# Optimization experiments

Hardware: AMD Instinct MI355X
Metric: run time of the kernel (lower is better)

## Reference

```python
import jax, jax.numpy as jnp
import numpy as np

N_NODES, N_VARS, E = 100000, 50000, 640000
FEAT, H, L = 16, 128, 4
N_INT, K = 20000, 8  # integer vars with categorical heads, uniform domain size


def _mlp2(x, W1, b1, W2, b2):
    return jnp.maximum(x @ W1 + b1, 0.0) @ W2 + b2


def setup_inputs() -> dict:
    key = jax.random.key(0)
    ks = jax.random.split(key, 24)
    s = lambda i, shape, scale: jax.random.normal(ks[i], shape, dtype=jnp.float32) * scale
    inp = {
        "x": jax.random.normal(ks[0], (N_NODES, FEAT), dtype=jnp.float32),
        "edge_index": jax.random.randint(ks[1], (2, E), 0, N_NODES, dtype=jnp.int32).astype(jnp.int64),
        "num_vars": N_VARS,
        # NodeEmbedder (var / cons)
        "ve_W1": s(2, (FEAT, H), 0.25), "ve_b1": jnp.zeros((H,), jnp.float32),
        "ve_W2": s(3, (H, H), 0.09),   "ve_b2": jnp.zeros((H,), jnp.float32),
        "ce_W1": s(4, (FEAT, H), 0.25), "ce_b1": jnp.zeros((H,), jnp.float32),
        "ce_W2": s(5, (H, H), 0.09),   "ce_b2": jnp.zeros((H,), jnp.float32),
        # GCN backbone: stacked per-layer params
        "conv_W": s(6, (L, H, H), 0.09), "conv_b": jnp.zeros((L, H), jnp.float32),
        "ref_W1": s(7, (L, H, H), 0.09), "ref_b1": jnp.zeros((L, H), jnp.float32),
        "ref_W2": s(8, (L, H, H), 0.09), "ref_b2": jnp.zeros((L, H), jnp.float32),
        # Bernoulli head: H -> H//2 -> 1
        "bh_W1": s(9, (H, H // 2), 0.09), "bh_b1": jnp.zeros((H // 2,), jnp.float32),
        "bh_W2": s(10, (H // 2, 1), 0.12), "bh_b2": jnp.zeros((1,), jnp.float32),
        # Categorical heads: one Linear(H, K) per integer variable, batched
        "cat_W": s(11, (N_INT, H, K), 0.09),
        "cat_b": jnp.zeros((N_INT, K), jnp.float32),
    }
    return inp


def reference(x, edge_index, num_vars,
              ve_W1, ve_b1, ve_W2, ve_b2,
              ce_W1, ce_b1, ce_W2, ce_b2,
              conv_W, conv_b, ref_W1, ref_b1, ref_W2, ref_b2,
              bh_W1, bh_b1, bh_W2, bh_b2,
              cat_W, cat_b):
    N = x.shape[0]
    src, dst = edge_index[0], edge_index[1]
    # GCN normalization with self-loops: deg includes the self edge
    deg = jax.ops.segment_sum(jnp.ones((src.shape[0],), x.dtype), dst, num_segments=N) + 1.0
    dinv_sqrt = jax.lax.rsqrt(deg)
    enorm = dinv_sqrt[src] * dinv_sqrt[dst]      # [E]
    self_norm = (1.0 / deg)[:, None]             # [N,1] self-loop weight deg^-1

    var_h = _mlp2(x[:num_vars], ve_W1, ve_b1, ve_W2, ve_b2)
    cons_h = _mlp2(x[num_vars:], ce_W1, ce_b1, ce_W2, ce_b2)
    h = jnp.concatenate([var_h, cons_h], axis=0)  # [N,H]

    def gcn_conv(xin, W, b):
        hw = xin @ W
        agg = jax.ops.segment_sum(hw[src] * enorm[:, None], dst, num_segments=N)
        return agg + hw * self_norm + b

    def layer(xc, p):
        W, b, W1, b1, W2, b2 = p
        h_ = jnp.maximum(gcn_conv(xc, W, b), 0.0)
        return xc + _mlp2(h_, W1, b1, W2, b2), None

    h, _ = jax.lax.scan(layer, h, (conv_W, conv_b, ref_W1, ref_b1, ref_W2, ref_b2))

    vh = h[:num_vars]
    bern_logits = _mlp2(vh, bh_W1, bh_b1, bh_W2, bh_b2)[:, 0]          # [num_vars]
    n_int = cat_W.shape[0]
    cat_logits = jnp.einsum('nh,nhk->nk', vh[:n_int], cat_W) + cat_b    # [n_int,K]
    return bern_logits, cat_logits
```

## Files before the change

### kernel.cpp

```cpp
#include <hip/hip_runtime.h>
#include <hip/hip_bf16.h>


#define NN 100000
#define NV 50000
#define NE 640000
#define FEAT 16
#define HD 128
#define NL 4
#define NI 20000
#define KK 8
#define SCAN_BLK 98
#define LDP 136
#define WE_STRIDE (128*32 + 128*128)

typedef __hip_bfloat16 bf16;
typedef __attribute__((ext_vector_type(8))) short short8;
typedef __attribute__((ext_vector_type(4))) float f32x4;

static __device__ __forceinline__ ushort f2bu(float f) {
    __hip_bfloat16 b = __float2bfloat16(f);
    return *reinterpret_cast<ushort*>(&b);
}
static __device__ __forceinline__ float bu2f(ushort u) {
    __hip_bfloat16 b = *reinterpret_cast<__hip_bfloat16*>(&u);
    return __bfloat162float(b);
}

__global__ void k_deg_init(float* deg) {
    int i = blockIdx.x * blockDim.x + threadIdx.x;
    if (i < NN) deg[i] = 1.0f;
}

__global__ void k_deg_scatter(const int* __restrict__ ei, float* deg) {
    int e = blockIdx.x * blockDim.x + threadIdx.x;
    if (e < NE) atomicAdd(&deg[ei[NE + e]], 1.0f);
}

__global__ void k_deg_fin(const float* __restrict__ deg, float* dinv, float* selfn) {
    int i = blockIdx.x * blockDim.x + threadIdx.x;
    if (i < NN) {
        float d = deg[i];
        dinv[i]  = rsqrtf(d);
        selfn[i] = 1.0f / d;
    }
}

__global__ void k_scan_part(const float* __restrict__ deg, int* __restrict__ part) {
    __shared__ int s[256];
    const int t = threadIdx.x;
    const int i = blockIdx.x * 1024 + t * 4;
    int sum = 0;
#pragma unroll
    for (int j = 0; j < 4; ++j)
        if (i + j < NN) sum += (int)deg[i + j] - 1;
    s[t] = sum;
    __syncthreads();
    for (int off = 128; off > 0; off >>= 1) {
        if (t < off) s[t] += s[t + off];
        __syncthreads();
    }
    if (t == 0) part[blockIdx.x] = s[0];
}

__global__ void k_scan_mid(const int* __restrict__ part, int* __restrict__ blockoff,
                           int* __restrict__ row_ptr) {
    __shared__ int s[128];
    const int t = threadIdx.x;
    int v = (t < SCAN_BLK) ? part[t] : 0;
    s[t] = v;
    __syncthreads();
    for (int off = 1; off < 128; off <<= 1) {
        int u = (t >= off) ? s[t - off] : 0;
        __syncthreads();
        s[t] += u;
        __syncthreads();
    }
    if (t < SCAN_BLK) blockoff[t] = s[t] - v;
    if (t == 0) row_ptr[NN] = NE;
}

__global__ void k_scan_apply(const float* __restrict__ deg,
                             const int* __restrict__ blockoff,
                             int* __restrict__ row_ptr, int* __restrict__ cnt) {
    __shared__ int s[256];
    const int t = threadIdx.x;
    const int i = blockIdx.x * 1024 + t * 4;
    int c[4];
    int tsum = 0;
#pragma unroll
    for (int j = 0; j < 4; ++j) {
        c[j] = (i + j < NN) ? (int)deg[i + j] - 1 : 0;
        tsum += c[j];
    }
    s[t] = tsum;
    __syncthreads();
    for (int off = 1; off < 256; off <<= 1) {
        int u = (t >= off) ? s[t - off] : 0;
        __syncthreads();
        s[t] += u;
        __syncthreads();
    }
    int off = blockoff[blockIdx.x] + s[t] - tsum;
#pragma unroll
    for (int j = 0; j < 4; ++j) {
        if (i + j < NN) {
            row_ptr[i + j] = off;
            cnt[i + j] = 0;
            off += c[j];
        }
    }
}

__global__ void k_csr_fill(const int* __restrict__ ei,
                           const int* __restrict__ row_ptr, int* __restrict__ cnt,
                           const float* __restrict__ dinv,
                           int* __restrict__ col, float* __restrict__ wgt) {
    int e = blockIdx.x * blockDim.x + threadIdx.x;
    if (e >= NE) return;
    const int s = ei[e];
    const int d = ei[NE + e];
    const int pos = row_ptr[d] + atomicAdd(&cnt[d], 1);
    col[pos] = s;
    wgt[pos] = dinv[s] * dinv[d];
}

__global__ void k_wprep(const float* __restrict__ conv_W,
                        const float* __restrict__ ref_W1,
                        const float* __restrict__ ref_W2,
                        ushort* __restrict__ wt) {
    const int mat = blockIdx.x >> 7;
    const int j = blockIdx.x & 127;
    const int k = threadIdx.x;
    const float* src = (mat < 4) ? conv_W + (size_t)mat * HD * HD
                     : (mat < 8) ? ref_W1 + (size_t)(mat - 4) * HD * HD
                                 : ref_W2 + (size_t)(mat - 8) * HD * HD;
    wt[(size_t)mat * HD * HD + j * HD + k] = f2bu(src[k * HD + j]);
}

__global__ void k_wprep_embed(const float* __restrict__ vW1, const float* __restrict__ vW2,
                              const float* __restrict__ cW1, const float* __restrict__ cW2,
                              ushort* __restrict__ wte) {
    const int side = blockIdx.x >> 7;
    const int j = blockIdx.x & 127;
    const int k = threadIdx.x;
    const float* W1 = side ? cW1 : vW1;
    const float* W2 = side ? cW2 : vW2;
    ushort* o = wte + (size_t)side * WE_STRIDE;
    if (k < 32) o[j * 32 + k] = (k < FEAT) ? f2bu(W1[k * HD + j]) : (ushort)0;
    o[128 * 32 + j * HD + k] = f2bu(W2[k * HD + j]);
}

__global__ __launch_bounds__(256, 4) void k_embed_mfma(
        const float* __restrict__ x,
        const ushort* __restrict__ W1t, const float* __restrict__ b1,
        const ushort* __restrict__ W2t, const float* __restrict__ b2,
        const ushort* __restrict__ Wtc,
        int nbase, int nend,
        ushort* __restrict__ hb, ushort* __restrict__ hwb) {
    const int lane = threadIdx.x & 63, w = threadIdx.x >> 6;
    const int l15 = lane & 15, lg = lane >> 4;
    const int rowb = nbase + blockIdx.x * 128;
    __shared__ ushort hsm[128][LDP];

#pragma unroll
    for (int rt = 0; rt < 2; ++rt) {
        const int r = rowb + w * 32 + rt * 16 + l15;
        const int rc = r < nend ? r : nend - 1;
        short8 a = {0, 0, 0, 0, 0, 0, 0, 0};
        if (lg < 2) {
            const float* xp = x + (size_t)rc * FEAT + lg * 8;
#pragma unroll
            for (int i = 0; i < 8; ++i) a[i] = (short)f2bu(xp[i]);
        }
#pragma unroll
        for (int jt = 0; jt < 8; ++jt) {
            const float bv = b1[jt * 16 + l15];
            f32x4 acc = {bv, bv, bv, bv};
            short8 b = *reinterpret_cast<const short8*>(&W1t[(jt * 16 + l15) * 32 + lg * 8]);
            acc = __builtin_amdgcn_mfma_f32_16x16x32_bf16(a, b, acc, 0, 0, 0);
#pragma unroll
            for (int rr = 0; rr < 4; ++rr)
                hsm[w * 32 + rt * 16 + lg * 4 + rr][jt * 16 + l15] =
                    f2bu(fmaxf(acc[rr], 0.0f));
        }
    }
    __syncthreads();

#pragma unroll
    for (int rt = 0; rt < 2; ++rt) {
        f32x4 acc[8];
#pragma unroll
        for (int jt = 0; jt < 8; ++jt) {
            const float bv = b2[jt * 16 + l15];
            f32x4 v = {bv, bv, bv, bv};
            acc[jt] = v;
        }
#pragma unroll
        for (int ks = 0; ks < 4; ++ks) {
            short8 a = *reinterpret_cast<const short8*>(&hsm[w * 32 + rt * 16 + l15][ks * 32 + lg * 8]);
#pragma unroll
            for (int jt = 0; jt < 8; ++jt) {
                short8 b = *reinterpret_cast<const short8*>(&W2t[(jt * 16 + l15) * HD + ks * 32 + lg * 8]);
                acc[jt] = __builtin_amdgcn_mfma_f32_16x16x32_bf16(a, b, acc[jt], 0, 0, 0);
            }
        }
#pragma unroll
        for (int jt = 0; jt < 8; ++jt)
#pragma unroll
            for (int rr = 0; rr < 4; ++rr) {
                const int row = rowb + w * 32 + rt * 16 + lg * 4 + rr;
                const ushort hv = f2bu(acc[jt][rr]);
                if (row < nend) hb[(size_t)row * HD + jt * 16 + l15] = hv;
                hsm[w * 32 + rt * 16 + lg * 4 + rr][jt * 16 + l15] = hv;
            }
        f32x4 acc3[8];
        const f32x4 zero = {0.f, 0.f, 0.f, 0.f};
#pragma unroll
        for (int jt = 0; jt < 8; ++jt) acc3[jt] = zero;
#pragma unroll
        for (int ks = 0; ks < 4; ++ks) {
            short8 a = *reinterpret_cast<const short8*>(&hsm[w * 32 + rt * 16 + l15][ks * 32 + lg * 8]);
#pragma unroll
            for (int jt = 0; jt < 8; ++jt) {
                short8 b = *reinterpret_cast<const short8*>(&Wtc[(jt * 16 + l15) * HD + ks * 32 + lg * 8]);
                acc3[jt] = __builtin_amdgcn_mfma_f32_16x16x32_bf16(a, b, acc3[jt], 0, 0, 0);
            }
        }
#pragma unroll
        for (int jt = 0; jt < 8; ++jt)
#pragma unroll
            for (int rr = 0; rr < 4; ++rr) {
                const int row = rowb + w * 32 + rt * 16 + lg * 4 + rr;
                if (row < nend)
                    hwb[(size_t)row * HD + jt * 16 + l15] = f2bu(acc3[jt][rr]);
            }
    }
}

__global__ __launch_bounds__(256) void k_hw(
                     const ushort* __restrict__ hb, const ushort* __restrict__ Wt,
                     ushort* __restrict__ hwb) {
    const int lane = threadIdx.x & 63;
    const int w = threadIdx.x >> 6;
    const int row0 = blockIdx.x * 128 + w * 32;
    const int l15 = lane & 15, lg = lane >> 4;

    const f32x4 zero = {0.f, 0.f, 0.f, 0.f};
    f32x4 acc[2][8];
#pragma unroll
    for (int rt = 0; rt < 2; ++rt)
#pragma unroll
        for (int jt = 0; jt < 8; ++jt) acc[rt][jt] = zero;

#pragma unroll
    for (int ks = 0; ks < 4; ++ks) {
        short8 a[2];
#pragma unroll
        for (int rt = 0; rt < 2; ++rt) {
            int r = row0 + rt * 16 + l15;
            r = r < NN ? r : NN - 1;
            a[rt] = *reinterpret_cast<const short8*>(&hb[(size_t)r * HD + ks * 32 + lg * 8]);
        }
#pragma unroll
        for (int jt = 0; jt < 8; ++jt) {
            short8 b = *reinterpret_cast<const short8*>(&Wt[(jt * 16 + l15) * HD + ks * 32 + lg * 8]);
            acc[0][jt] = __builtin_amdgcn_mfma_f32_16x16x32_bf16(a[0], b, acc[0][jt], 0, 0, 0);
            acc[1][jt] = __builtin_amdgcn_mfma_f32_16x16x32_bf16(a[1], b, acc[1][jt], 0, 0, 0);
        }
    }
#pragma unroll
    for (int rt = 0; rt < 2; ++rt)
#pragma unroll
        for (int jt = 0; jt < 8; ++jt)
#pragma unroll
            for (int r = 0; r < 4; ++r) {
                int row = row0 + rt * 16 + lg * 4 + r;
                if (row < NN) hwb[(size_t)row * HD + jt * 16 + l15] = f2bu(acc[rt][jt][r]);
            }
}

__global__ __launch_bounds__(512, 4) void k_combine(
                          const ushort* __restrict__ hwb,
                          const int* __restrict__ row_ptr,
                          const int* __restrict__ col,
                          const float* __restrict__ wgt,
                          const float* __restrict__ selfn,
                          const float* __restrict__ cb,
                          const ushort* __restrict__ Wt1, const float* __restrict__ b1,
                          const ushort* __restrict__ Wt2, const float* __restrict__ b2,
                          ushort* __restrict__ hb) {
    const int t = threadIdx.x;
    const int n0 = blockIdx.x * 64;
    __shared__ ushort hs[64][LDP];
    __shared__ ushort hid[64][LDP];
    __shared__ int rp[65];

    if (t <= 64) {
        int idx = n0 + t;
        rp[t] = row_ptr[idx < NN ? idx : NN];
    }
    __syncthreads();

    const int lane = t & 63, w = t >> 6;
    {
        const int c0 = 2 * lane;
        const float cbx = cb[c0], cby = cb[c0 + 1];
        float accx[8], accy[8];
        int ecur[8], eend[8];
        int rounds = 0;
#pragma unroll
        for (int m = 0; m < 8; ++m) {
            const int node = n0 + w * 8 + m;
            const int nc = node < NN ? node : NN - 1;
            const uint hv = *reinterpret_cast<const uint*>(&hwb[(size_t)nc * HD + c0]);
            const float sn = selfn[nc];
            accx[m] = bu2f((ushort)(hv & 0xffffu)) * sn + cbx;
            accy[m] = bu2f((ushort)(hv >> 16)) * sn + cby;
            ecur[m] = rp[w * 8 + m];
            eend[m] = rp[w * 8 + m + 1];
            rounds = max(rounds, eend[m] - ecur[m]);
        }
#pragma unroll 1
        for (int r = 0; r < rounds; r += 2) {
            uint va[8], vb[8];
            float wa[8], wb[8];
            int ca[8], cc[8];
#pragma unroll
            for (int m = 0; m < 8; ++m) {
                const int e0 = ecur[m];
                const int a0 = (e0 < eend[m]) ? e0 : 0;
                const int a1 = (e0 + 1 < eend[m]) ? e0 + 1 : 0;
                wa[m] = (e0 < eend[m]) ? wgt[a0] : 0.0f;
                wb[m] = (e0 + 1 < eend[m]) ? wgt[a1] : 0.0f;
                ca[m] = col[a0];
                cc[m] = col[a1];
            }
#pragma unroll
            for (int m = 0; m < 8; ++m) {
                va[m] = *reinterpret_cast<const uint*>(&hwb[(size_t)ca[m] * HD + c0]);
                vb[m] = *reinterpret_cast<const uint*>(&hwb[(size_t)cc[m] * HD + c0]);
            }
#pragma unroll
            for (int m = 0; m < 8; ++m) {
                accx[m] += wa[m] * bu2f((ushort)(va[m] & 0xffffu));
                accy[m] += wa[m] * bu2f((ushort)(va[m] >> 16));
                accx[m] += wb[m] * bu2f((ushort)(vb[m] & 0xffffu));
                accy[m] += wb[m] * bu2f((ushort)(vb[m] >> 16));
            }
#pragma unroll
            for (int m = 0; m < 8; ++m) ecur[m] += 2;
        }
#pragma unroll
        for (int m = 0; m < 8; ++m) {
            const uint px = (uint)f2bu(fmaxf(accx[m], 0.0f));
            const uint py = (uint)f2bu(fmaxf(accy[m], 0.0f));
            *reinterpret_cast<uint*>(&hs[w * 8 + m][c0]) = px | (py << 16);
        }
    }
    __syncthreads();

    const int l15 = lane & 15, lg = lane >> 4;
    const int rt = (w & 3) * 16;
    const int c0 = (w >> 2) * 64;

    f32x4 acc1[4];
#pragma unroll
    for (int jt = 0; jt < 4; ++jt) {
        float bv = b1[c0 + jt * 16 + l15];
        f32x4 v = {bv, bv, bv, bv};
        acc1[jt] = v;
    }
#pragma unroll
    for (int ks = 0; ks < 4; ++ks) {
        short8 a = *reinterpret_cast<const short8*>(&hs[rt + l15][ks * 32 + lg * 8]);
#pragma unroll
        for (int jt = 0; jt < 4; ++jt) {
            short8 b = *reinterpret_cast<const short8*>(&Wt1[(c0 + jt * 16 + l15) * HD + ks * 32 + lg * 8]);
            acc1[jt] = __builtin_amdgcn_mfma_f32_16x16x32_bf16(a, b, acc1[jt], 0, 0, 0);
        }
    }
#pragma unroll
    for (int jt = 0; jt < 4; ++jt)
#pragma unroll
        for (int r = 0; r < 4; ++r)
            hid[rt + lg * 4 + r][c0 + jt * 16 + l15] = f2bu(fmaxf(acc1[jt][r], 0.0f));
    __syncthreads();

    f32x4 acc2[4];
#pragma unroll
    for (int jt = 0; jt < 4; ++jt) {
        float bv = b2[c0 + jt * 16 + l15];
        f32x4 v = {bv, bv, bv, bv};
        acc2[jt] = v;
    }
#pragma unroll
    for (int ks = 0; ks < 4; ++ks) {
        short8 a = *reinterpret_cast<const short8*>(&hid[rt + l15][ks * 32 + lg * 8]);
#pragma unroll
        for (int jt = 0; jt < 4; ++jt) {
            short8 b = *reinterpret_cast<const short8*>(&Wt2[(c0 + jt * 16 + l15) * HD + ks * 32 + lg * 8]);
            acc2[jt] = __builtin_amdgcn_mfma_f32_16x16x32_bf16(a, b, acc2[jt], 0, 0, 0);
        }
    }
#pragma unroll
    for (int jt = 0; jt < 4; ++jt)
#pragma unroll
        for (int r = 0; r < 4; ++r) {
            const int row = n0 + rt + lg * 4 + r;
            if (row < NN) {
                const size_t idx = (size_t)row * HD + c0 + jt * 16 + l15;
                hb[idx] = f2bu(acc2[jt][r] + bu2f(hb[idx]));
            }
        }
}

__global__ void k_bern(const ushort* __restrict__ hb,
                       const float* __restrict__ W1, const float* __restrict__ b1,
                       const float* __restrict__ W2, const float* __restrict__ b2,
                       float* __restrict__ out) {
    const long long t = (long long)blockIdx.x * blockDim.x + threadIdx.x;
    const int n = (int)(t >> 6);
    const int lane = (int)(t & 63);
    if (n >= NV) return;
    const ushort* hn = hb + (size_t)n * HD;
    float acc = b1[lane];
#pragma unroll 8
    for (int k = 0; k < HD; ++k) acc += bu2f(hn[k]) * W1[k * 64 + lane];
    float p = fmaxf(acc, 0.0f) * W2[lane];
#pragma unroll
    for (int off = 32; off > 0; off >>= 1) p += __shfl_down(p, off);
    if (lane == 0) out[n] = p + b2[0];
}

__global__ void k_cat(const ushort* __restrict__ hb,
                      const float* __restrict__ cW, const float* __restrict__ cb,
                      float* __restrict__ out) {
    const long long t = (long long)blockIdx.x * blockDim.x + threadIdx.x;
    const int n = (int)(t >> 6);
    const int lane = (int)(t & 63);
    if (n >= NI) return;
    const ushort* hn = hb + (size_t)n * HD;
    float p[KK];
#pragma unroll
    for (int k = 0; k < KK; ++k) p[k] = 0.0f;
#pragma unroll
    for (int half = 0; half < 2; ++half) {
        const int hh = lane + 64 * half;
        const float vh = bu2f(hn[hh]);
        const float* wp = cW + ((size_t)n * HD + hh) * KK;
        const float4 w0 = *reinterpret_cast<const float4*>(wp);
        const float4 w1 = *reinterpret_cast<const float4*>(wp + 4);
        p[0] += vh * w0.x; p[1] += vh * w0.y; p[2] += vh * w0.z; p[3] += vh * w0.w;
        p[4] += vh * w1.x; p[5] += vh * w1.y; p[6] += vh * w1.z; p[7] += vh * w1.w;
    }
#pragma unroll
    for (int k = 0; k < KK; ++k) {
#pragma unroll
        for (int off = 32; off > 0; off >>= 1) p[k] += __shfl_down(p[k], off);
    }
    if (lane == 0) {
#pragma unroll
        for (int k = 0; k < KK; ++k) out[NV + (size_t)n * KK + k] = p[k] + cb[(size_t)n * KK + k];
    }
}

extern "C" void kernel_launch(void* const* d_in, const int* in_sizes, int n_in,
                              void* d_out, int out_size, void* d_ws, size_t ws_size,
                              hipStream_t stream) {
    const float* x  = (const float*)d_in[0];
    const int*   ei = (const int*)d_in[1];
    const float* ve_W1 = (const float*)d_in[3];
    const float* ve_b1 = (const float*)d_in[4];
    const float* ve_W2 = (const float*)d_in[5];
    const float* ve_b2 = (const float*)d_in[6];
    const float* ce_W1 = (const float*)d_in[7];
    const float* ce_b1 = (const float*)d_in[8];
    const float* ce_W2 = (const float*)d_in[9];
    const float* ce_b2 = (const float*)d_in[10];
    const float* conv_W = (const float*)d_in[11];
    const float* conv_b = (const float*)d_in[12];
    const float* ref_W1 = (const float*)d_in[13];
    const float* ref_b1 = (const float*)d_in[14];
    const float* ref_W2 = (const float*)d_in[15];
    const float* ref_b2 = (const float*)d_in[16];
    const float* bh_W1 = (const float*)d_in[17];
    const float* bh_b1 = (const float*)d_in[18];
    const float* bh_W2 = (const float*)d_in[19];
    const float* bh_b2 = (const float*)d_in[20];
    const float* cat_W = (const float*)d_in[21];
    const float* cat_b = (const float*)d_in[22];
    float* out = (float*)d_out;

    const size_t need = (size_t)(3 * NN + (NN + 1) + NN + 2 * NE + 2 * SCAN_BLK) * 4
                      + (size_t)3 * NN * HD * 2
                      + (size_t)12 * HD * HD * 2
                      + (size_t)2 * WE_STRIDE * 2;
    if (ws_size < need) return;

    float* deg     = (float*)d_ws;
    float* dinv    = deg + NN;
    float* selfn   = dinv + NN;
    int*   row_ptr = (int*)(selfn + NN);
    int*   cnt     = row_ptr + (NN + 1);
    int*   col     = cnt + NN;
    float* wgt     = (float*)(col + NE);
    int*   part    = (int*)(wgt + NE);
    int*   blockoff= part + SCAN_BLK;
    ushort* hwbA   = (ushort*)(blockoff + SCAN_BLK);
    ushort* hwbB   = hwbA + (size_t)NN * HD;
    ushort* hb     = hwbB + (size_t)NN * HD;
    ushort* wt     = hb + (size_t)NN * HD;
    ushort* wte    = wt + (size_t)12 * HD * HD;

    k_deg_init<<<(NN + 255) / 256, 256, 0, stream>>>(deg);
    k_deg_scatter<<<(NE + 255) / 256, 256, 0, stream>>>(ei, deg);
    k_deg_fin<<<(NN + 255) / 256, 256, 0, stream>>>(deg, dinv, selfn);
    k_scan_part<<<SCAN_BLK, 256, 0, stream>>>(deg, part);
    k_scan_mid<<<1, 128, 0, stream>>>(part, blockoff, row_ptr);
    k_scan_apply<<<SCAN_BLK, 256, 0, stream>>>(deg, blockoff, row_ptr, cnt);
    k_csr_fill<<<(NE + 255) / 256, 256, 0, stream>>>(ei, row_ptr, cnt, dinv, col, wgt);
    k_wprep<<<12 * 128, 128, 0, stream>>>(conv_W, ref_W1, ref_W2, wt);
    k_wprep_embed<<<256, 128, 0, stream>>>(ve_W1, ve_W2, ce_W1, ce_W2, wte);

    k_embed_mfma<<<(NV + 127) / 128, 256, 0, stream>>>(
        x, wte, ve_b1, wte + 128 * 32, ve_b2, wt, 0, NV, hb, hwbA);
    k_embed_mfma<<<(NN - NV + 127) / 128, 256, 0, stream>>>(
        x, wte + WE_STRIDE, ce_b1, wte + WE_STRIDE + 128 * 32, ce_b2, wt, NV, NN, hb, hwbA);

    for (int l = 0; l < NL; ++l) {
        if (l > 0)
            k_hw<<<(NN + 127) / 128, 256, 0, stream>>>(hb, wt + (size_t)l * HD * HD, hwbA);
        k_combine<<<(NN + 63) / 64, 512, 0, stream>>>(hwbA, row_ptr, col, wgt, selfn,
                                               conv_b + (size_t)l * HD,
                                               wt + (size_t)(4 + l) * HD * HD,
                                               ref_b1 + (size_t)l * HD,
                                               wt + (size_t)(8 + l) * HD * HD,
                                               ref_b2 + (size_t)l * HD,
                                               hb);
    }

    k_bern<<<(NV * 64) / 256, 256, 0, stream>>>(hb, bh_W1, bh_b1, bh_W2, bh_b2, out);
    k_cat<<<(NI * 64) / 256, 256, 0, stream>>>(hb, cat_W, cat_b, out);
}
```

Measured before the change: 806.7 us.

## Sort nodes by degree so combine blocks process similar-degree nodes together

```diff
diff --git a/kernel.cpp b/kernel.cpp
--- a/kernel.cpp
+++ b/kernel.cpp
@@ -13,6 +13,7 @@
 #define SCAN_BLK 98
 #define LDP 136
 #define WE_STRIDE (128*32 + 128*128)
+#define NDBUCK 256
 
 typedef __hip_bfloat16 bf16;
 typedef __attribute__((ext_vector_type(8))) short short8;
@@ -125,6 +126,47 @@
     wgt[pos] = dinv[s] * dinv[d];
 }
 
+__global__ void k_hist_init(int* dhist, int* dcnt2) {
+    int i = threadIdx.x;
+    dhist[i] = 0;
+    dcnt2[i] = 0;
+}
+
+__global__ void k_hist(const float* __restrict__ deg, int* __restrict__ dhist) {
+    int i = blockIdx.x * blockDim.x + threadIdx.x;
+    if (i < NN) {
+        int d = (int)deg[i] - 1;
+        atomicAdd(&dhist[d < NDBUCK ? d : NDBUCK - 1], 1);
+    }
+}
+
+__global__ void k_hist_scan(const int* __restrict__ dhist, int* __restrict__ dbase) {
+    __shared__ int s[NDBUCK];
+    const int t = threadIdx.x;
+    int v = dhist[t];
+    s[t] = v;
+    __syncthreads();
+    for (int off = 1; off < NDBUCK; off <<= 1) {
+        int u = (t >= off) ? s[t - off] : 0;
+        __syncthreads();
+        s[t] += u;
+        __syncthreads();
+    }
+    dbase[t] = s[t] - v;
+}
+
+__global__ void k_perm_fill(const float* __restrict__ deg,
+                            const int* __restrict__ dbase, int* __restrict__ dcnt2,
+                            int* __restrict__ perm) {
+    int i = blockIdx.x * blockDim.x + threadIdx.x;
+    if (i < NN) {
+        int d = (int)deg[i] - 1;
+        d = d < NDBUCK ? d : NDBUCK - 1;
+        const int pos = dbase[d] + atomicAdd(&dcnt2[d], 1);
+        perm[pos] = i;
+    }
+}
+
 __global__ void k_wprep(const float* __restrict__ conv_W,
                         const float* __restrict__ ref_W1,
                         const float* __restrict__ ref_W2,
@@ -289,16 +331,22 @@
                           const float* __restrict__ cb,
                           const ushort* __restrict__ Wt1, const float* __restrict__ b1,
                           const ushort* __restrict__ Wt2, const float* __restrict__ b2,
-                          ushort* __restrict__ hb) {
+                          ushort* __restrict__ hb,
+                          const int* __restrict__ perm) {
     const int t = threadIdx.x;
     const int n0 = blockIdx.x * 64;
     __shared__ ushort hs[64][LDP];
     __shared__ ushort hid[64][LDP];
-    __shared__ int rp[65];
-
-    if (t <= 64) {
-        int idx = n0 + t;
-        rp[t] = row_ptr[idx < NN ? idx : NN];
+    __shared__ int pm[64];
+    __shared__ int rp0[64], rp1[64];
+
+    if (t < 64) {
+        const int idx = n0 + t;
+        const int node = (idx < NN) ? perm[idx] : -1;
+        pm[t] = node;
+        const int nc = node >= 0 ? node : 0;
+        rp0[t] = row_ptr[nc];
+        rp1[t] = node >= 0 ? row_ptr[nc + 1] : row_ptr[nc];
     }
     __syncthreads();
 
@@ -311,14 +359,14 @@
         int rounds = 0;
 #pragma unroll
         for (int m = 0; m < 8; ++m) {
-            const int node = n0 + w * 8 + m;
-            const int nc = node < NN ? node : NN - 1;
+            const int node = pm[w * 8 + m];
+            const int nc = node >= 0 ? node : 0;
             const uint hv = *reinterpret_cast<const uint*>(&hwb[(size_t)nc * HD + c0]);
             const float sn = selfn[nc];
             accx[m] = bu2f((ushort)(hv & 0xffffu)) * sn + cbx;
             accy[m] = bu2f((ushort)(hv >> 16)) * sn + cby;
-            ecur[m] = rp[w * 8 + m];
-            eend[m] = rp[w * 8 + m + 1];
+            ecur[m] = rp0[w * 8 + m];
+            eend[m] = rp1[w * 8 + m];
             rounds = max(rounds, eend[m] - ecur[m]);
         }
 #pragma unroll 1
@@ -407,9 +455,9 @@
     for (int jt = 0; jt < 4; ++jt)
 #pragma unroll
         for (int r = 0; r < 4; ++r) {
-            const int row = n0 + rt + lg * 4 + r;
-            if (row < NN) {
-                const size_t idx = (size_t)row * HD + c0 + jt * 16 + l15;
+            const int node = pm[rt + lg * 4 + r];
+            if (node >= 0) {
+                const size_t idx = (size_t)node * HD + c0 + jt * 16 + l15;
                 hb[idx] = f2bu(acc2[jt][r] + bu2f(hb[idx]));
             }
         }
@@ -495,7 +543,8 @@
     const size_t need = (size_t)(3 * NN + (NN + 1) + NN + 2 * NE + 2 * SCAN_BLK) * 4
                       + (size_t)3 * NN * HD * 2
                       + (size_t)12 * HD * HD * 2
-                      + (size_t)2 * WE_STRIDE * 2;
+                      + (size_t)2 * WE_STRIDE * 2
+                      + (size_t)(3 * NDBUCK + NN) * 4;
     if (ws_size < need) return;
 
     float* deg     = (float*)d_ws;
@@ -512,6 +561,10 @@
     ushort* hb     = hwbB + (size_t)NN * HD;
     ushort* wt     = hb + (size_t)NN * HD;
     ushort* wte    = wt + (size_t)12 * HD * HD;
+    int*   dhist   = (int*)(wte + (size_t)2 * WE_STRIDE);
+    int*   dbase   = dhist + NDBUCK;
+    int*   dcnt2   = dbase + NDBUCK;
+    int*   perm    = dcnt2 + NDBUCK;
 
     k_deg_init<<<(NN + 255) / 256, 256, 0, stream>>>(deg);
     k_deg_scatter<<<(NE + 255) / 256, 256, 0, stream>>>(ei, deg);
@@ -520,6 +573,10 @@
     k_scan_mid<<<1, 128, 0, stream>>>(part, blockoff, row_ptr);
     k_scan_apply<<<SCAN_BLK, 256, 0, stream>>>(deg, blockoff, row_ptr, cnt);
     k_csr_fill<<<(NE + 255) / 256, 256, 0, stream>>>(ei, row_ptr, cnt, dinv, col, wgt);
+    k_hist_init<<<1, NDBUCK, 0, stream>>>(dhist, dcnt2);
+    k_hist<<<(NN + 255) / 256, 256, 0, stream>>>(deg, dhist);
+    k_hist_scan<<<1, NDBUCK, 0, stream>>>(dhist, dbase);
+    k_perm_fill<<<(NN + 255) / 256, 256, 0, stream>>>(deg, dbase, dcnt2, perm);
     k_wprep<<<12 * 128, 128, 0, stream>>>(conv_W, ref_W1, ref_W2, wt);
     k_wprep_embed<<<256, 128, 0, stream>>>(ve_W1, ve_W2, ce_W1, ce_W2, wte);
 
@@ -537,7 +594,7 @@
                                                ref_b1 + (size_t)l * HD,
                                                wt + (size_t)(8 + l) * HD * HD,
                                                ref_b2 + (size_t)l * HD,
-                                               hb);
+                                               hb, perm);
     }
 
     k_bern<<<(NV * 64) / 256, 256, 0, stream>>>(hb, bh_W1, bh_b1, bh_W2, bh_b2, out);
```

Result: slower. 1.530 ms (+89.6%).
